# Optimization experiments

Hardware: AMD Instinct MI355X
Metric: run time of the kernel (lower is better)

## Reference

```python
import jax, jax.numpy as jnp
import numpy as np

N_NODES = 50000


def gcn_conv(h, src, dst, W, b, n):
    # PyG GCNConv: x' = D^{-1/2} (A + I) D^{-1/2} (h W) + b
    x = h @ W  # [N, out]
    deg = jax.ops.segment_sum(jnp.ones_like(src, dtype=x.dtype), dst, num_segments=n) + 1.0  # self-loop
    dis = deg ** -0.5
    norm = dis[src] * dis[dst]  # [E]
    msg = x[src] * norm[:, None]  # [E, out]
    agg = jax.ops.segment_sum(msg, dst, num_segments=n)
    agg = agg + x * (dis * dis)[:, None]  # self-loop term: 1/deg_i * x_i
    return agg + b


def setup_inputs() -> dict:
    key = jax.random.key(0)
    ks = jax.random.split(key, 8)
    n, e = N_NODES, 800000
    d_in, d_rni, h = 128, 32, 256
    x = jax.random.normal(ks[0], (n, d_in), dtype=jnp.float32)
    rni = jax.random.normal(ks[1], (n, d_rni), dtype=jnp.float32)
    edge_index = jax.random.randint(ks[2], (2, e), 0, n, dtype=jnp.int64)
    s1 = (d_in + d_rni) ** -0.5
    s2 = h ** -0.5
    W1 = jax.random.normal(ks[3], (d_in + d_rni, h), dtype=jnp.float32) * s1
    b1 = jnp.zeros((h,), dtype=jnp.float32)
    W2 = jax.random.normal(ks[4], (h, h), dtype=jnp.float32) * s2
    b2 = jnp.zeros((h,), dtype=jnp.float32)
    W_out = jax.random.normal(ks[5], (h, h), dtype=jnp.float32) * s2
    b_out = jnp.zeros((h,), dtype=jnp.float32)
    return {"x": x, "rni": rni, "edge_index": edge_index, "W1": W1, "b1": b1,
            "W2": W2, "b2": b2, "W_out": W_out, "b_out": b_out}


def reference(x, rni, edge_index, W1, b1, W2, b2, W_out, b_out):
    n = x.shape[0]
    src, dst = edge_index[0], edge_index[1]
    h = jnp.concatenate([x, rni], axis=-1)  # RNI concat
    h = jax.nn.relu(gcn_conv(h, src, dst, W1, b1, n))
    h = jax.nn.relu(gcn_conv(h, src, dst, W2, b2, n))
    return h @ W_out + b_out
```

## Files before the change

kernel.cpp:

```cpp
#include <hip/hip_runtime.h>
#include <hip/hip_bf16.h>
#include <hip/hip_fp16.h>
#include <math.h>

#define D_IN   128
#define D_RNI  32
#define HID    256

typedef _Float16 half8 __attribute__((ext_vector_type(8)));
typedef float    f32x4 __attribute__((ext_vector_type(4)));

__global__ void k_detect(const unsigned int* __restrict__ w, int nwords, int* __restrict__ mode) {
    __shared__ unsigned int red[256];
    unsigned int acc = 0;
    for (int i = threadIdx.x; i < 1024; i += 256) {
        int idx = 2 * i + 1;
        if (idx < nwords) acc |= w[idx];
    }
    red[threadIdx.x] = acc;
    __syncthreads();
    for (int s = 128; s > 0; s >>= 1) {
        if (threadIdx.x < s) red[threadIdx.x] |= red[threadIdx.x + s];
        __syncthreads();
    }
    if (threadIdx.x == 0) *mode = (red[0] == 0u) ? 1 : 0;
}

__global__ void k_count(const unsigned int* __restrict__ ew, const int* __restrict__ mode_p,
                        int* __restrict__ counts, int e) {
    int mode = *mode_p;
    int i = blockIdx.x * 256 + threadIdx.x;
    if (i >= e) return;
    int d = mode ? (int)ew[2 * ((size_t)e + i)] : (int)ew[(size_t)e + i];
    atomicAdd(&counts[d], 1);
}

__global__ __launch_bounds__(1024) void k_scan1(const int* __restrict__ counts,
                                                int* __restrict__ incl,
                                                int* __restrict__ bsum, int n) {
    __shared__ int sd[1024];
    int t = threadIdx.x;
    int i = blockIdx.x * 1024 + t;
    int v = (i < n) ? counts[i] : 0;
    sd[t] = v;
    __syncthreads();
    for (int off = 1; off < 1024; off <<= 1) {
        int tmp = (t >= off) ? sd[t - off] : 0;
        __syncthreads();
        sd[t] += tmp;
        __syncthreads();
    }
    if (i < n) incl[i] = sd[t];
    if (t == 1023) bsum[blockIdx.x] = sd[1023];
}

__global__ __launch_bounds__(1024) void k_scan2(int* __restrict__ bsum, int nb) {
    __shared__ int sd[1024];
    int t = threadIdx.x;
    int v = (t < nb) ? bsum[t] : 0;
    sd[t] = v;
    __syncthreads();
    for (int off = 1; off < 1024; off <<= 1) {
        int tmp = (t >= off) ? sd[t - off] : 0;
        __syncthreads();
        sd[t] += tmp;
        __syncthreads();
    }
    if (t < nb) bsum[t] = sd[t] - v;
    if (t == nb - 1) bsum[nb] = sd[t];
}

__global__ void k_scan3(const int* __restrict__ counts, const int* __restrict__ incl,
                        const int* __restrict__ bsum,
                        int* __restrict__ rowptr, int* __restrict__ cursor,
                        float* __restrict__ dis, int n, int nb) {
    int i = blockIdx.x * 256 + threadIdx.x;
    if (i >= n) return;
    int excl = incl[i] - counts[i] + bsum[i >> 10];
    rowptr[i] = excl;
    cursor[i] = excl;
    dis[i] = 1.0f / sqrtf((float)(counts[i] + 1));
    if (i == 0) rowptr[n] = bsum[nb];
}

__global__ void k_scatter(const unsigned int* __restrict__ ew, const int* __restrict__ mode_p,
                          int* __restrict__ cursor, int* __restrict__ csr, int e) {
    int mode = *mode_p;
    int i = blockIdx.x * 256 + threadIdx.x;
    if (i >= e) return;
    int s, d;
    if (mode) {
        s = (int)ew[2 * (size_t)i];
        d = (int)ew[2 * ((size_t)e + i)];
    } else {
        s = (int)ew[(size_t)i];
        d = (int)ew[(size_t)e + i];
    }
    int pos = atomicAdd(&cursor[d], 1);
    csr[pos] = s;
}

__global__ void k_cvt_cols(const float* __restrict__ src, int w4, __half* __restrict__ dst,
                           int dstw, int off, int total4) {
    int i = blockIdx.x * 256 + threadIdx.x;
    if (i >= total4) return;
    int row = i / w4;
    int c4 = (i - row * w4) * 4;
    float4 v = reinterpret_cast<const float4*>(src)[i];
    union { __half h[4]; float2 f2; } u;
    u.h[0] = __float2half(v.x); u.h[1] = __float2half(v.y);
    u.h[2] = __float2half(v.z); u.h[3] = __float2half(v.w);
    *reinterpret_cast<float2*>(&dst[(size_t)row * dstw + off + c4]) = u.f2;
}

__global__ void k_cvt_wt(const float* __restrict__ W, __half* __restrict__ Wt,
                         int K, int N, int total) {
    int i = blockIdx.x * 256 + threadIdx.x;
    if (i >= total) return;
    int k = i / N, nn = i - k * N;
    Wt[(size_t)nn * K + k] = __float2half(W[i]);
}

#define KT 32
#define LSTR 40
template <bool ADD_BIAS, bool HALF_OUT>
__global__ __launch_bounds__(256) void k_mgemm(const __half* __restrict__ A,
                                               const __half* __restrict__ Bt,
                                               const float* __restrict__ bias,
                                               void* Cv, int M, int K) {
    __shared__ __half As[64 * LSTR];
    __shared__ __half Bs[256 * LSTR];
    int tid = threadIdx.x;
    int wave = tid >> 6, lane = tid & 63;
    int q = lane >> 4, m16 = lane & 15;
    int r0 = blockIdx.x * 64;

    f32x4 acc[4][4] = {};

    for (int k0 = 0; k0 < K; k0 += KT) {
        __syncthreads();
        {
            int r = tid >> 2, kq = (tid & 3) * 8;
            int row = r0 + r; if (row >= M) row = M - 1;
            uint4 v = *reinterpret_cast<const uint4*>(&A[(size_t)row * K + k0 + kq]);
            *reinterpret_cast<uint4*>(&As[r * LSTR + kq]) = v;
        }
        {
            int nb = tid >> 2, kq = (tid & 3) * 8;
            #pragma unroll
            for (int i = 0; i < 4; ++i) {
                int nn = nb + i * 64;
                uint4 v = *reinterpret_cast<const uint4*>(&Bt[(size_t)nn * K + k0 + kq]);
                *reinterpret_cast<uint4*>(&Bs[nn * LSTR + kq]) = v;
            }
        }
        __syncthreads();

        half8 af[4], bf[4];
        #pragma unroll
        for (int mi = 0; mi < 4; ++mi)
            af[mi] = *reinterpret_cast<const half8*>(&As[(mi * 16 + m16) * LSTR + q * 8]);
        #pragma unroll
        for (int ni = 0; ni < 4; ++ni)
            bf[ni] = *reinterpret_cast<const half8*>(&Bs[(wave * 64 + ni * 16 + m16) * LSTR + q * 8]);
        #pragma unroll
        for (int mi = 0; mi < 4; ++mi)
            #pragma unroll
            for (int ni = 0; ni < 4; ++ni)
                acc[mi][ni] = __builtin_amdgcn_mfma_f32_16x16x32_f16(af[mi], bf[ni], acc[mi][ni], 0, 0, 0);
    }

    #pragma unroll
    for (int mi = 0; mi < 4; ++mi) {
        #pragma unroll
        for (int r = 0; r < 4; ++r) {
            int row = r0 + mi * 16 + q * 4 + r;
            if (row >= M) continue;
            #pragma unroll
            for (int ni = 0; ni < 4; ++ni) {
                int col = wave * 64 + ni * 16 + m16;
                float v = acc[mi][ni][r];
                if (ADD_BIAS) v += bias[col];
                if (HALF_OUT) ((__half*)Cv)[(size_t)row * HID + col] = __float2half(v);
                else          ((float*)Cv)[(size_t)row * HID + col] = v;
            }
        }
    }
}

__global__ __launch_bounds__(128) void k_agg(const __half2* __restrict__ xh,
                                             const int* __restrict__ rowptr,
                                             const int* __restrict__ csr,
                                             const float* __restrict__ dis,
                                             const float* __restrict__ bias,
                                             __half2* __restrict__ outh, int n) {
    int i = blockIdx.x;
    int c = threadIdx.x;
    float disd = dis[i];
    int e0 = rowptr[i], e1 = rowptr[i + 1];
    float2 self = __half22float2(xh[(size_t)i * 128 + c]);
    float acc0 = self.x * disd * disd;
    float acc1 = self.y * disd * disd;

    __shared__ int   s_idx[128];
    __shared__ float s_w[128];
    for (int e = e0; e < e1; e += 128) {
        int cnt = min(128, e1 - e);
        __syncthreads();
        if (c < cnt) {
            int s = csr[e + c];
            s_idx[c] = s;
            s_w[c] = dis[s] * disd;
        }
        __syncthreads();
        int j = 0;
        for (; j + 4 <= cnt; j += 4) {
            float2 f0 = __half22float2(xh[(size_t)s_idx[j + 0] * 128 + c]);
            float2 f1 = __half22float2(xh[(size_t)s_idx[j + 1] * 128 + c]);
            float2 f2 = __half22float2(xh[(size_t)s_idx[j + 2] * 128 + c]);
            float2 f3 = __half22float2(xh[(size_t)s_idx[j + 3] * 128 + c]);
            acc0 = fmaf(f0.x, s_w[j + 0], acc0); acc1 = fmaf(f0.y, s_w[j + 0], acc1);
            acc0 = fmaf(f1.x, s_w[j + 1], acc0); acc1 = fmaf(f1.y, s_w[j + 1], acc1);
            acc0 = fmaf(f2.x, s_w[j + 2], acc0); acc1 = fmaf(f2.y, s_w[j + 2], acc1);
            acc0 = fmaf(f3.x, s_w[j + 3], acc0); acc1 = fmaf(f3.y, s_w[j + 3], acc1);
        }
        for (; j < cnt; ++j) {
            float2 f = __half22float2(xh[(size_t)s_idx[j] * 128 + c]);
            acc0 = fmaf(f.x, s_w[j], acc0);
            acc1 = fmaf(f.y, s_w[j], acc1);
        }
    }
    acc0 = fmaxf(acc0 + bias[2 * c + 0], 0.0f);
    acc1 = fmaxf(acc1 + bias[2 * c + 1], 0.0f);
    outh[(size_t)i * 128 + c] = __floats2half2_rn(acc0, acc1);
}

extern "C" void kernel_launch(void* const* d_in, const int* in_sizes, int n_in,
                              void* d_out, int out_size, void* d_ws, size_t ws_size,
                              hipStream_t stream) {
    const float* x     = (const float*)d_in[0];
    const float* rni   = (const float*)d_in[1];
    const unsigned int* ew = (const unsigned int*)d_in[2];
    const float* W1    = (const float*)d_in[3];
    const float* b1    = (const float*)d_in[4];
    const float* W2    = (const float*)d_in[5];
    const float* b2    = (const float*)d_in[6];
    const float* W_out = (const float*)d_in[7];
    const float* b_out = (const float*)d_in[8];
    float* out = (float*)d_out;

    const int n  = in_sizes[0] / D_IN;
    const int e  = in_sizes[2] / 2;
    const int nb = (n + 1023) / 1024;
    const int K1 = D_IN + D_RNI;

    char* ws = (char*)d_ws;
    size_t off = 0;
    auto carve = [&](size_t bytes) {
        char* p = ws + off;
        off = (off + bytes + 255) & ~(size_t)255;
        return p;
    };
    __half* xcat  = (__half*)carve((size_t)n * K1 * sizeof(__half));
    __half* xh    = (__half*)carve((size_t)n * HID * sizeof(__half));
    __half* h     = (__half*)carve((size_t)n * HID * sizeof(__half));
    __half* W1t   = (__half*)carve((size_t)K1 * HID * sizeof(__half));
    __half* W2t   = (__half*)carve((size_t)HID * HID * sizeof(__half));
    __half* Wot   = (__half*)carve((size_t)HID * HID * sizeof(__half));
    int*   counts = (int*)carve((size_t)n * sizeof(int));
    int*   incl   = (int*)carve((size_t)n * sizeof(int));
    int*   bsum   = (int*)carve((size_t)(nb + 1) * sizeof(int));
    int*   rowptr = (int*)carve((size_t)(n + 1) * sizeof(int));
    int*   cursor = (int*)carve((size_t)n * sizeof(int));
    float* dis    = (float*)carve((size_t)n * sizeof(float));
    int*   csr    = (int*)carve((size_t)e * sizeof(int));
    int*   mode   = (int*)carve(sizeof(int));
    (void)ws_size;

    const int eb = (e + 255) / 256;
    const int gemm_blocks = (n + 63) / 64;

    k_detect<<<1, 256, 0, stream>>>(ew, 2 * e, mode);
    hipMemsetAsync(counts, 0, (size_t)n * sizeof(int), stream);
    k_count<<<eb, 256, 0, stream>>>(ew, mode, counts, e);
    k_scan1<<<nb, 1024, 0, stream>>>(counts, incl, bsum, n);
    k_scan2<<<1, 1024, 0, stream>>>(bsum, nb);
    k_scan3<<<(n + 255) / 256, 256, 0, stream>>>(counts, incl, bsum, rowptr, cursor, dis, n, nb);
    k_scatter<<<eb, 256, 0, stream>>>(ew, mode, cursor, csr, e);

    {
        int t1 = n * (D_IN / 4);
        k_cvt_cols<<<(t1 + 255) / 256, 256, 0, stream>>>(x, D_IN / 4, xcat, K1, 0, t1);
        int t2 = n * (D_RNI / 4);
        k_cvt_cols<<<(t2 + 255) / 256, 256, 0, stream>>>(rni, D_RNI / 4, xcat, K1, D_IN, t2);
        int tw1 = K1 * HID;
        k_cvt_wt<<<(tw1 + 255) / 256, 256, 0, stream>>>(W1, W1t, K1, HID, tw1);
        int tw = HID * HID;
        k_cvt_wt<<<(tw + 255) / 256, 256, 0, stream>>>(W2, W2t, HID, HID, tw);
        k_cvt_wt<<<(tw + 255) / 256, 256, 0, stream>>>(W_out, Wot, HID, HID, tw);
    }

    k_mgemm<false, true><<<gemm_blocks, 256, 0, stream>>>(xcat, W1t, nullptr, xh, n, K1);
    k_agg<<<n, 128, 0, stream>>>((const __half2*)xh, rowptr, csr, dis, b1, (__half2*)h, n);

    k_mgemm<false, true><<<gemm_blocks, 256, 0, stream>>>(h, W2t, nullptr, xh, n, HID);
    k_agg<<<n, 128, 0, stream>>>((const __half2*)xh, rowptr, csr, dis, b2, (__half2*)h, n);

    k_mgemm<true, false><<<gemm_blocks, 256, 0, stream>>>(h, Wot, b_out, out, n, HID);
}
```

Baseline: 409.4 us.

## Fuse input concat/convert into first GEMM and use wave-per-node aggregation

Drops the separate fp32-to-fp16 concat kernels and has the first GEMM read x and rni directly as fp32, converting to half while staging the A tile. This removes a full write and re-read of the concatenated input. The aggregation kernel now gives each node one 64-lane wave with 4 channels per lane. Neighbor indices and weights are broadcast with shuffles instead of shared memory plus block barriers, and four nodes share a 256-thread block. The trade-off is doubled fp32 A-tile load traffic in GEMM1 and wider per-lane gathers.

Result: faster. 390.4 us (-4.7%).

```diff
diff --git a/kernel.cpp b/kernel.cpp
--- a/kernel.cpp
+++ b/kernel.cpp
@@ -100,19 +100,6 @@
     csr[pos] = s;
 }
 
-__global__ void k_cvt_cols(const float* __restrict__ src, int w4, __half* __restrict__ dst,
-                           int dstw, int off, int total4) {
-    int i = blockIdx.x * 256 + threadIdx.x;
-    if (i >= total4) return;
-    int row = i / w4;
-    int c4 = (i - row * w4) * 4;
-    float4 v = reinterpret_cast<const float4*>(src)[i];
-    union { __half h[4]; float2 f2; } u;
-    u.h[0] = __float2half(v.x); u.h[1] = __float2half(v.y);
-    u.h[2] = __float2half(v.z); u.h[3] = __float2half(v.w);
-    *reinterpret_cast<float2*>(&dst[(size_t)row * dstw + off + c4]) = u.f2;
-}
-
 __global__ void k_cvt_wt(const float* __restrict__ W, __half* __restrict__ Wt,
                          int K, int N, int total) {
     int i = blockIdx.x * 256 + threadIdx.x;
@@ -123,8 +110,9 @@
 
 #define KT 32
 #define LSTR 40
-template <bool ADD_BIAS, bool HALF_OUT>
-__global__ __launch_bounds__(256) void k_mgemm(const __half* __restrict__ A,
+template <bool A_F32, bool ADD_BIAS, bool HALF_OUT>
+__global__ __launch_bounds__(256) void k_mgemm(const void* __restrict__ Av, int strideA, int KA,
+                                               const void* __restrict__ A2v, int strideA2,
                                                const __half* __restrict__ Bt,
                                                const float* __restrict__ bias,
                                                void* Cv, int M, int K) {
@@ -142,8 +130,24 @@
         {
             int r = tid >> 2, kq = (tid & 3) * 8;
             int row = r0 + r; if (row >= M) row = M - 1;
-            uint4 v = *reinterpret_cast<const uint4*>(&A[(size_t)row * K + k0 + kq]);
-            *reinterpret_cast<uint4*>(&As[r * LSTR + kq]) = v;
+            if (A_F32) {
+                const float* src; int stride, kk0;
+                if (k0 < KA) { src = (const float*)Av;  stride = strideA;  kk0 = k0; }
+                else         { src = (const float*)A2v; stride = strideA2; kk0 = k0 - KA; }
+                const float* p = &src[(size_t)row * stride + kk0 + kq];
+                float4 va = *reinterpret_cast<const float4*>(p);
+                float4 vb = *reinterpret_cast<const float4*>(p + 4);
+                union { __half2 h2[4]; uint4 u; } uu;
+                uu.h2[0] = __floats2half2_rn(va.x, va.y);
+                uu.h2[1] = __floats2half2_rn(va.z, va.w);
+                uu.h2[2] = __floats2half2_rn(vb.x, vb.y);
+                uu.h2[3] = __floats2half2_rn(vb.z, vb.w);
+                *reinterpret_cast<uint4*>(&As[r * LSTR + kq]) = uu.u;
+            } else {
+                const __half* src = (const __half*)Av;
+                uint4 v = *reinterpret_cast<const uint4*>(&src[(size_t)row * strideA + k0 + kq]);
+                *reinterpret_cast<uint4*>(&As[r * LSTR + kq]) = v;
+            }
         }
         {
             int nb = tid >> 2, kq = (tid & 3) * 8;
@@ -188,51 +192,78 @@
     }
 }
 
-__global__ __launch_bounds__(128) void k_agg(const __half2* __restrict__ xh,
+__global__ __launch_bounds__(256) void k_agg(const __half* __restrict__ xh,
                                              const int* __restrict__ rowptr,
                                              const int* __restrict__ csr,
                                              const float* __restrict__ dis,
                                              const float* __restrict__ bias,
-                                             __half2* __restrict__ outh, int n) {
-    int i = blockIdx.x;
-    int c = threadIdx.x;
+                                             __half* __restrict__ outh, int n) {
+    int i = blockIdx.x * 4 + (threadIdx.x >> 6);
+    if (i >= n) return;
+    int lane = threadIdx.x & 63;
+    int c4 = lane * 4;
     float disd = dis[i];
     int e0 = rowptr[i], e1 = rowptr[i + 1];
-    float2 self = __half22float2(xh[(size_t)i * 128 + c]);
-    float acc0 = self.x * disd * disd;
-    float acc1 = self.y * disd * disd;
-
-    __shared__ int   s_idx[128];
-    __shared__ float s_w[128];
-    for (int e = e0; e < e1; e += 128) {
-        int cnt = min(128, e1 - e);
-        __syncthreads();
-        if (c < cnt) {
-            int s = csr[e + c];
-            s_idx[c] = s;
-            s_w[c] = dis[s] * disd;
-        }
-        __syncthreads();
+
+    float acc0, acc1, acc2, acc3;
+    {
+        uint2 v = *reinterpret_cast<const uint2*>(&xh[(size_t)i * HID + c4]);
+        float2 f0 = __half22float2(*reinterpret_cast<__half2*>(&v.x));
+        float2 f1 = __half22float2(*reinterpret_cast<__half2*>(&v.y));
+        float ws = disd * disd;
+        acc0 = f0.x * ws; acc1 = f0.y * ws; acc2 = f1.x * ws; acc3 = f1.y * ws;
+    }
+
+    for (int e = e0; e < e1; e += 64) {
+        int cnt = min(64, e1 - e);
+        int sreg = 0; float wreg = 0.0f;
+        if (lane < cnt) {
+            sreg = csr[e + lane];
+            wreg = dis[sreg] * disd;
+        }
         int j = 0;
         for (; j + 4 <= cnt; j += 4) {
-            float2 f0 = __half22float2(xh[(size_t)s_idx[j + 0] * 128 + c]);
-            float2 f1 = __half22float2(xh[(size_t)s_idx[j + 1] * 128 + c]);
-            float2 f2 = __half22float2(xh[(size_t)s_idx[j + 2] * 128 + c]);
-            float2 f3 = __half22float2(xh[(size_t)s_idx[j + 3] * 128 + c]);
-            acc0 = fmaf(f0.x, s_w[j + 0], acc0); acc1 = fmaf(f0.y, s_w[j + 0], acc1);
-            acc0 = fmaf(f1.x, s_w[j + 1], acc0); acc1 = fmaf(f1.y, s_w[j + 1], acc1);
-            acc0 = fmaf(f2.x, s_w[j + 2], acc0); acc1 = fmaf(f2.y, s_w[j + 2], acc1);
-            acc0 = fmaf(f3.x, s_w[j + 3], acc0); acc1 = fmaf(f3.y, s_w[j + 3], acc1);
+            int   s0 = __shfl(sreg, j + 0), s1 = __shfl(sreg, j + 1);
+            int   s2 = __shfl(sreg, j + 2), s3 = __shfl(sreg, j + 3);
+            float w0 = __shfl(wreg, j + 0), w1 = __shfl(wreg, j + 1);
+            float w2 = __shfl(wreg, j + 2), w3 = __shfl(wreg, j + 3);
+            uint2 v0 = *reinterpret_cast<const uint2*>(&xh[(size_t)s0 * HID + c4]);
+            uint2 v1 = *reinterpret_cast<const uint2*>(&xh[(size_t)s1 * HID + c4]);
+            uint2 v2 = *reinterpret_cast<const uint2*>(&xh[(size_t)s2 * HID + c4]);
+            uint2 v3 = *reinterpret_cast<const uint2*>(&xh[(size_t)s3 * HID + c4]);
+            float2 a0 = __half22float2(*reinterpret_cast<__half2*>(&v0.x));
+            float2 b0 = __half22float2(*reinterpret_cast<__half2*>(&v0.y));
+            float2 a1 = __half22float2(*reinterpret_cast<__half2*>(&v1.x));
+            float2 b1 = __half22float2(*reinterpret_cast<__half2*>(&v1.y));
+            float2 a2 = __half22float2(*reinterpret_cast<__half2*>(&v2.x));
+            float2 b2 = __half22float2(*reinterpret_cast<__half2*>(&v2.y));
+            float2 a3 = __half22float2(*reinterpret_cast<__half2*>(&v3.x));
+            float2 b3 = __half22float2(*reinterpret_cast<__half2*>(&v3.y));
+            acc0 = fmaf(a0.x, w0, acc0); acc1 = fmaf(a0.y, w0, acc1);
+            acc2 = fmaf(b0.x, w0, acc2); acc3 = fmaf(b0.y, w0, acc3);
+            acc0 = fmaf(a1.x, w1, acc0); acc1 = fmaf(a1.y, w1, acc1);
+            acc2 = fmaf(b1.x, w1, acc2); acc3 = fmaf(b1.y, w1, acc3);
+            acc0 = fmaf(a2.x, w2, acc0); acc1 = fmaf(a2.y, w2, acc1);
+            acc2 = fmaf(b2.x, w2, acc2); acc3 = fmaf(b2.y, w2, acc3);
+            acc0 = fmaf(a3.x, w3, acc0); acc1 = fmaf(a3.y, w3, acc1);
+            acc2 = fmaf(b3.x, w3, acc2); acc3 = fmaf(b3.y, w3, acc3);
         }
         for (; j < cnt; ++j) {
-            float2 f = __half22float2(xh[(size_t)s_idx[j] * 128 + c]);
-            acc0 = fmaf(f.x, s_w[j], acc0);
-            acc1 = fmaf(f.y, s_w[j], acc1);
-        }
-    }
-    acc0 = fmaxf(acc0 + bias[2 * c + 0], 0.0f);
-    acc1 = fmaxf(acc1 + bias[2 * c + 1], 0.0f);
-    outh[(size_t)i * 128 + c] = __floats2half2_rn(acc0, acc1);
+            int   s = __shfl(sreg, j);
+            float w = __shfl(wreg, j);
+            uint2 v = *reinterpret_cast<const uint2*>(&xh[(size_t)s * HID + c4]);
+            float2 a = __half22float2(*reinterpret_cast<__half2*>(&v.x));
+            float2 b = __half22float2(*reinterpret_cast<__half2*>(&v.y));
+            acc0 = fmaf(a.x, w, acc0); acc1 = fmaf(a.y, w, acc1);
+            acc2 = fmaf(b.x, w, acc2); acc3 = fmaf(b.y, w, acc3);
+        }
+    }
+
+    float4 bb = *reinterpret_cast<const float4*>(&bias[c4]);
+    union { __half2 h2[2]; uint2 u; } o;
+    o.h2[0] = __floats2half2_rn(fmaxf(acc0 + bb.x, 0.0f), fmaxf(acc1 + bb.y, 0.0f));
+    o.h2[1] = __floats2half2_rn(fmaxf(acc2 + bb.z, 0.0f), fmaxf(acc3 + bb.w, 0.0f));
+    *reinterpret_cast<uint2*>(&outh[(size_t)i * HID + c4]) = o.u;
 }
 
 extern "C" void kernel_launch(void* const* d_in, const int* in_sizes, int n_in,
@@ -261,7 +292,6 @@
         off = (off + bytes + 255) & ~(size_t)255;
         return p;
     };
-    __half* xcat  = (__half*)carve((size_t)n * K1 * sizeof(__half));
     __half* xh    = (__half*)carve((size_t)n * HID * sizeof(__half));
     __half* h     = (__half*)carve((size_t)n * HID * sizeof(__half));
     __half* W1t   = (__half*)carve((size_t)K1 * HID * sizeof(__half));
@@ -279,6 +309,7 @@
 
     const int eb = (e + 255) / 256;
     const int gemm_blocks = (n + 63) / 64;
+    const int agg_blocks  = (n + 3) / 4;
 
     k_detect<<<1, 256, 0, stream>>>(ew, 2 * e, mode);
     hipMemsetAsync(counts, 0, (size_t)n * sizeof(int), stream);
@@ -289,10 +320,6 @@
     k_scatter<<<eb, 256, 0, stream>>>(ew, mode, cursor, csr, e);
 
     {
-        int t1 = n * (D_IN / 4);
-        k_cvt_cols<<<(t1 + 255) / 256, 256, 0, stream>>>(x, D_IN / 4, xcat, K1, 0, t1);
-        int t2 = n * (D_RNI / 4);
-        k_cvt_cols<<<(t2 + 255) / 256, 256, 0, stream>>>(rni, D_RNI / 4, xcat, K1, D_IN, t2);
         int tw1 = K1 * HID;
         k_cvt_wt<<<(tw1 + 255) / 256, 256, 0, stream>>>(W1, W1t, K1, HID, tw1);
         int tw = HID * HID;
@@ -300,11 +327,14 @@
         k_cvt_wt<<<(tw + 255) / 256, 256, 0, stream>>>(W_out, Wot, HID, HID, tw);
     }
 
-    k_mgemm<false, true><<<gemm_blocks, 256, 0, stream>>>(xcat, W1t, nullptr, xh, n, K1);
-    k_agg<<<n, 128, 0, stream>>>((const __half2*)xh, rowptr, csr, dis, b1, (__half2*)h, n);
-
-    k_mgemm<false, true><<<gemm_blocks, 256, 0, stream>>>(h, W2t, nullptr, xh, n, HID);
-    k_agg<<<n, 128, 0, stream>>>((const __half2*)xh, rowptr, csr, dis, b2, (__half2*)h, n);
-
-    k_mgemm<true, false><<<gemm_blocks, 256, 0, stream>>>(h, Wot, b_out, out, n, HID);
-}
+    k_mgemm<true, false, true><<<gemm_blocks, 256, 0, stream>>>(x, D_IN, D_IN, rni, D_RNI,
+                                                                W1t, nullptr, xh, n, K1);
+    k_agg<<<agg_blocks, 256, 0, stream>>>(xh, rowptr, csr, dis, b1, h, n);
+
+    k_mgemm<false, false, true><<<gemm_blocks, 256, 0, stream>>>(h, HID, HID, nullptr, 0,
+                                                                 W2t, nullptr, xh, n, HID);
+    k_agg<<<agg_blocks, 256, 0, stream>>>(xh, rowptr, csr, dis, b2, h, n);
+
+    k_mgemm<false, true, false><<<gemm_blocks, 256, 0, stream>>>(h, HID, HID, nullptr, 0,
+                                                                 Wot, b_out, out, n, HID);
+}
```
